# Performance work log

Measured on AMD Instinct MI355X. Metric: run time of the kernel, lower is better.

The kernel has to match this reference:

```python
import jax, jax.numpy as jnp
import numpy as np

DIM, QK, GS, DEPTH, VOCAB, ROT = 16, 128, 256, 8, 1024, 32
EPS = 1e-5


def scale_norm(x, g):
    # ScaleNorm: x / max(||x|| * dim^-0.5, eps) * g
    norm = jnp.linalg.norm(x, axis=-1, keepdims=True) * (DIM ** -0.5)
    return x / jnp.clip(norm, EPS) * g


def rotate_half(x):
    # interleaved pairs: (x0,x1,x2,x3,...) -> (-x1,x0,-x3,x2,...)
    xr = x.reshape(x.shape[:-1] + (-1, 2))
    a, b = xr[..., 0], xr[..., 1]
    return jnp.stack((-b, a), axis=-1).reshape(x.shape)


def apply_rotary(x, cos, sin):
    # rotary applied to first ROT dims only
    xr, xp = x[..., :ROT], x[..., ROT:]
    return jnp.concatenate([xr * cos + rotate_half(xr) * sin, xp], axis=-1)


def flash_layer(x, p, cos, sin, keymask, n):
    b = x.shape[0]
    normed = scale_norm(x, p['norm_g'])
    # shift_tokens: first half of channels shifted forward by one position
    xs, xp = jnp.split(normed, 2, axis=-1)
    xs = jnp.pad(xs, ((0, 0), (1, 0), (0, 0)))[:, :-1]
    normed = jnp.concatenate([xs, xp], axis=-1)
    hid = jax.nn.silu(normed @ p['Wh'] + p['bh'])  # [b,n,64]
    v, gate = jnp.split(hid, 2, axis=-1)           # each [b,n,32]
    qk = jax.nn.silu(normed @ p['Wqk'] + p['bqk'])  # [b,n,128]
    offs = qk[..., None, :] * p['gamma'] + p['beta']  # [b,n,4,128]
    quad_q, lin_q, quad_k, lin_k = [apply_rotary(offs[..., i, :], cos, sin) for i in range(4)]
    pad = (-n) % GS
    grp = lambda t: jnp.pad(t, ((0, 0), (0, pad), (0, 0))).reshape(b, -1, GS, t.shape[-1])
    quad_q, quad_k, lin_q, lin_k, vg = map(grp, (quad_q, quad_k, lin_q, lin_k, v))
    # quadratic (local, within-group) attention with ReLU^2
    sim = jnp.einsum('bgid,bgjd->bgij', quad_q, quad_k) / GS
    attn = jnp.square(jax.nn.relu(sim)) * keymask  # mask out padded keys
    quad_out = jnp.einsum('bgij,bgjd->bgid', attn, vg)
    # linear (global, across-group) attention, reduced over groups
    lin_kv = jnp.einsum('bgnd,bgne->bde', lin_k, vg) / n
    lin_out = jnp.einsum('bgnd,bde->bgne', lin_q, lin_kv)
    out = (quad_out + lin_out).reshape(b, -1, v.shape[-1])[:, :n]
    out = gate * out
    return out @ p['Wo'] + p['bo'] + x


def forward(kmer_data, token_emb, pos_scale, norm_g, Wh, bh, Wqk, bqk, gamma, beta, Wo, bo, final_g, Wl, bl, W1, b1, W2, b2):
    b, n = kmer_data.shape
    x = token_emb[kmer_data]  # [b,n,16]
    t = jnp.arange(n, dtype=jnp.float32)
    # ScaledSinuEmbedding
    inv = 1.0 / (10000.0 ** (jnp.arange(0, DIM, 2, dtype=jnp.float32) / DIM))
    sinu = t[:, None] * inv[None, :]
    pos = jnp.concatenate([jnp.sin(sinu), jnp.cos(sinu)], axis=-1) * pos_scale
    x = x + pos
    # rotary tables (dim 32, interleaved repeat)
    rinv = 1.0 / (10000.0 ** (jnp.arange(0, ROT, 2, dtype=jnp.float32) / ROT))
    rf = jnp.repeat(t[:, None] * rinv[None, :], 2, axis=-1)  # [n,32]
    cos, sin = jnp.cos(rf), jnp.sin(rf)
    # key mask for padded positions (996 -> 1024)
    pad = (-n) % GS
    keymask = jnp.pad(jnp.ones((n,), jnp.float32), (0, pad)).reshape(1, -1, 1, GS)
    for i in range(DEPTH):
        p = dict(norm_g=norm_g[i], Wh=Wh[i], bh=bh[i], Wqk=Wqk[i], bqk=bqk[i],
                 gamma=gamma[i], beta=beta[i], Wo=Wo[i], bo=bo[i])
        x = flash_layer(x, p, cos, sin, keymask, n)
    logits = scale_norm(x, final_g) @ Wl + bl  # [b,n,1024]
    h = jnp.max(logits, axis=-1)               # AdaptiveMaxPool1d(1) + Flatten -> [b,n]
    h = jax.nn.relu(h @ W1 + b1)
    return h @ W2 + b2                          # [b,1]


def setup_inputs() -> dict:
    key = jax.random.key(0)
    ks = jax.random.split(key, 12)
    r = lambda k, shape, s: jax.random.normal(k, shape, jnp.float32) * s
    return {
        'kmer_data': jax.random.randint(ks[0], (128, 996), 0, VOCAB),
        'token_emb': r(ks[1], (VOCAB, DIM), 1.0),
        'pos_scale': jnp.float32(1.0),
        'norm_g': jnp.ones((DEPTH,), jnp.float32),
        'Wh': r(ks[2], (DEPTH, DIM, 64), 0.1),
        'bh': jnp.zeros((DEPTH, 64), jnp.float32),
        'Wqk': r(ks[3], (DEPTH, DIM, QK), 0.1),
        'bqk': jnp.zeros((DEPTH, QK), jnp.float32),
        'gamma': 1.0 + r(ks[4], (DEPTH, 4, QK), 0.02),
        'beta': r(ks[5], (DEPTH, 4, QK), 0.02),
        'Wo': r(ks[6], (DEPTH, 32, DIM), 0.1),
        'bo': jnp.zeros((DEPTH, DIM), jnp.float32),
        'final_g': jnp.float32(1.0),
        'Wl': r(ks[7], (DIM, VOCAB), 0.1),
        'bl': jnp.zeros((VOCAB,), jnp.float32),
        'W1': r(ks[8], (996, 32), 0.05),
        'b1': jnp.zeros((32,), jnp.float32),
        'W2': r(ks[9], (32, 1), 0.1),
        'b2': jnp.zeros((1,), jnp.float32),
    }


def reference(kmer_data, token_emb, pos_scale, norm_g, Wh, bh, Wqk, bqk, gamma, beta, Wo, bo, final_g, Wl, bl, W1, b1, W2, b2):
    return forward(kmer_data, token_emb, pos_scale, norm_g, Wh, bh, Wqk, bqk,
                   gamma, beta, Wo, bo, final_g, Wl, bl, W1, b1, W2, b2)
```

## Files before the change

kernel.cpp:

```cpp
#include <hip/hip_runtime.h>

typedef short s16x8 __attribute__((ext_vector_type(8)));
typedef float f32x4 __attribute__((ext_vector_type(4)));

#define NB    128
#define NTOK  996
#define NPAD  1024
#define NGRP  4
#define GSZ   256
#define NLAY  8

__device__ __forceinline__ float bf2f(unsigned short u){
    unsigned int v = ((unsigned int)u) << 16;
    return __uint_as_float(v);
}
__device__ __forceinline__ unsigned short f2bf(float f){
    unsigned int x = __float_as_uint(f);
    unsigned int r = (x + 0x7fffu + ((x >> 16) & 1u)) >> 16;
    return (unsigned short)r;
}
__device__ __forceinline__ unsigned int packbf(float a, float b){
    return (unsigned int)f2bf(a) | ((unsigned int)f2bf(b) << 16);
}
__device__ __forceinline__ float silu(float v){
    return v / (1.0f + __expf(-v));
}

__device__ __forceinline__ s16x8 derive_core(const unsigned short* __restrict__ qrow, int d0,
        float4 g0, float4 g1, float4 b0, float4 b1,
        const float* __restrict__ rp, bool rot){
    uint4 u = *(const uint4*)(qrow + d0);
    float y0 = bf2f((unsigned short)(u.x & 0xffffu))*g0.x + b0.x;
    float y1 = bf2f((unsigned short)(u.x >> 16))    *g0.y + b0.y;
    float y2 = bf2f((unsigned short)(u.y & 0xffffu))*g0.z + b0.z;
    float y3 = bf2f((unsigned short)(u.y >> 16))    *g0.w + b0.w;
    float y4 = bf2f((unsigned short)(u.z & 0xffffu))*g1.x + b1.x;
    float y5 = bf2f((unsigned short)(u.z >> 16))    *g1.y + b1.y;
    float y6 = bf2f((unsigned short)(u.w & 0xffffu))*g1.z + b1.z;
    float y7 = bf2f((unsigned short)(u.w >> 16))    *g1.w + b1.w;
    if (rot){
        float4 c4 = *(const float4*)(rp);
        float4 s4 = *(const float4*)(rp + 16);
        float a;
        a = y0; y0 = a*c4.x - y1*s4.x; y1 = y1*c4.x + a*s4.x;
        a = y2; y2 = a*c4.y - y3*s4.y; y3 = y3*c4.y + a*s4.y;
        a = y4; y4 = a*c4.z - y5*s4.z; y5 = y5*c4.z + a*s4.z;
        a = y6; y6 = a*c4.w - y7*s4.w; y7 = y7*c4.w + a*s4.w;
    }
    union { unsigned int uu[4]; s16x8 s; } r;
    r.uu[0] = packbf(y0, y1);
    r.uu[1] = packbf(y2, y3);
    r.uu[2] = packbf(y4, y5);
    r.uu[3] = packbf(y6, y7);
    return r.s;
}

__global__ void k_rope(float* __restrict__ rope){
    int t = blockIdx.x * 256 + threadIdx.x;
    if (t >= NPAD) return;
    float tf = (float)t;
    #pragma unroll
    for (int i = 0; i < 16; i++){
        float inv = expf(((float)(2*i) / 32.0f) * -9.210340371976184f);
        float ang = tf * inv;
        rope[t*32 + i]      = cosf(ang);
        rope[t*32 + 16 + i] = sinf(ang);
    }
}

__global__ __launch_bounds__(256) void k_embed(const int* __restrict__ kmer,
                                               const float* __restrict__ emb,
                                               const float* __restrict__ ps,
                                               float* __restrict__ x){
    int gid = blockIdx.x * 256 + threadIdx.x;
    if (gid >= NB * NTOK) return;
    int b = gid / NTOK;
    int tt = gid - b * NTOK;
    int idx = kmer[gid];
    const float* er = emb + (size_t)idx * 16;
    float pscale = ps[0];
    float tf = (float)tt;
    float* xr = x + (size_t)gid * 16;
    #pragma unroll
    for (int i = 0; i < 8; i++){
        float inv = expf(((float)(2*i) / 16.0f) * -9.210340371976184f);
        float ang = tf * inv;
        xr[i]     = er[i]     + sinf(ang) * pscale;
        xr[8 + i] = er[8 + i] + cosf(ang) * pscale;
    }
}

__global__ __launch_bounds__(256) void k_padzero(unsigned short* __restrict__ vT){
    int rid = blockIdx.x * 256 + threadIdx.x;
    if (rid < NB * 32){
        unsigned int* vp = (unsigned int*)(vT + (size_t)rid * NPAD + NTOK);
        #pragma unroll
        for (int i = 0; i < 14; i++) vp[i] = 0u;
    }
}

__global__ __launch_bounds__(256) void k_pre(const float* __restrict__ x,
                                             const float* __restrict__ Wh, const float* __restrict__ bh,
                                             const float* __restrict__ Wqk, const float* __restrict__ bqk,
                                             const float* __restrict__ norm_g, int layer,
                                             unsigned short* __restrict__ qk,
                                             unsigned short* __restrict__ vT,
                                             unsigned short* __restrict__ gateb){
    __shared__ __align__(16) unsigned short WcT[192 * 40];
    __shared__ __align__(16) unsigned short As[256 * 40];
    int tid = threadIdx.x;
    const float* Whl = Wh  + (size_t)layer * 1024;
    const float* Wql = Wqk + (size_t)layer * 2048;
    for (int i = tid; i < 1024; i += 256){ int d = i >> 6, c = i & 63;  WcT[c*40 + d] = f2bf(Whl[i]); }
    for (int i = tid; i < 2048; i += 256){ int d = i >> 7, c = i & 127; WcT[(64 + c)*40 + d] = f2bf(Wql[i]); }
    if (tid < 192){
        int i = tid;
        float bv = (i < 64) ? bh[layer*64 + i] : bqk[layer*128 + (i - 64)];
        WcT[i*40 + 16] = f2bf(bv);
        WcT[i*40 + 17] = 0;
        unsigned int* zz = (unsigned int*)(WcT + i*40 + 18);
        #pragma unroll
        for (int k = 0; k < 7; k++) zz[k] = 0u;
    }
    int gid0 = blockIdx.x * 256;
    {
        int t = gid0 + tid;
        int b = t / NTOK, tt = t - b * NTOK;
        float g = norm_g[layer];
        const float4* xr4 = (const float4*)(x + (size_t)t * 16);
        float cur[16];
        float s2 = 0.f;
        #pragma unroll
        for (int c = 0; c < 4; c++){
            float4 v4 = xr4[c];
            cur[4*c] = v4.x; cur[4*c+1] = v4.y; cur[4*c+2] = v4.z; cur[4*c+3] = v4.w;
        }
        #pragma unroll
        for (int d = 0; d < 16; d++) s2 += cur[d]*cur[d];
        float sc = g / fmaxf(sqrtf(s2) * 0.25f, 1e-5f);
        float pv[8]; float sp = 0.f;
        #pragma unroll
        for (int d = 0; d < 8; d++) pv[d] = 0.f;
        if (tt > 0){
            const float4* xp4 = (const float4*)(x + (size_t)(t - 1) * 16);
            float prv[16]; float p2 = 0.f;
            #pragma unroll
            for (int c = 0; c < 4; c++){
                float4 v4 = xp4[c];
                prv[4*c] = v4.x; prv[4*c+1] = v4.y; prv[4*c+2] = v4.z; prv[4*c+3] = v4.w;
            }
            #pragma unroll
            for (int d = 0; d < 16; d++) p2 += prv[d]*prv[d];
            sp = g / fmaxf(sqrtf(p2) * 0.25f, 1e-5f);
            #pragma unroll
            for (int d = 0; d < 8; d++) pv[d] = prv[d];
        }
        unsigned int* dd = (unsigned int*)(As + tid * 40);
        #pragma unroll
        for (int i = 0; i < 4; i++) dd[i] = packbf(pv[2*i]*sp, pv[2*i+1]*sp);
        #pragma unroll
        for (int i = 0; i < 4; i++) dd[4 + i] = packbf(cur[8 + 2*i]*sc, cur[9 + 2*i]*sc);
        dd[8] = 0x00003f80u;
        #pragma unroll
        for (int i = 9; i < 16; i++) dd[i] = 0u;
    }
    __syncthreads();
    int w = tid >> 6, lane = tid & 63, m16 = lane & 15, quad = lane >> 4;
    s16x8 wf[12];
    #pragma unroll
    for (int mi = 0; mi < 12; mi++)
        wf[mi] = *(const s16x8*)(WcT + (mi*16 + m16)*40 + quad*8);
    f32x4 zacc = {0.f,0.f,0.f,0.f};
    #pragma unroll
    for (int nt = 0; nt < 4; nt++){
        int tloc = w*64 + nt*16 + m16;
        int t = gid0 + tloc;
        int b = t / NTOK, tt = t - b * NTOK;
        s16x8 bf = *(const s16x8*)(As + tloc*40 + quad*8);
        size_t rowq = ((size_t)b*NPAD + tt);
        #pragma unroll
        for (int mi = 0; mi < 12; mi++){
            f32x4 r = __builtin_amdgcn_mfma_f32_16x16x32_bf16(wf[mi], bf, zacc, 0, 0, 0);
            float sv[4];
            #pragma unroll
            for (int reg = 0; reg < 4; reg++) sv[reg] = silu(r[reg]);
            int wc0 = mi*16 + quad*4;
            if (mi < 2){
                #pragma unroll
                for (int reg = 0; reg < 4; reg++)
                    vT[((size_t)b*32 + wc0 + reg)*NPAD + tt] = f2bf(sv[reg]);
            } else if (mi < 4){
                *(uint2*)(gateb + rowq*32 + (wc0 - 32)) = make_uint2(packbf(sv[0],sv[1]), packbf(sv[2],sv[3]));
            } else {
                *(uint2*)(qk + rowq*128 + (wc0 - 64)) = make_uint2(packbf(sv[0],sv[1]), packbf(sv[2],sv[3]));
            }
        }
    }
}

__global__ __launch_bounds__(256) void k_linkv(const unsigned short* __restrict__ qk,
                                               const unsigned short* __restrict__ vT,
                                               const float* __restrict__ rope,
                                               const float* __restrict__ gamma, const float* __restrict__ beta,
                                               int layer, float* __restrict__ linkvp){
    __shared__ __align__(16) unsigned short LkT[2][128 * 40];
    int tid = threadIdx.x;
    int b = blockIdx.x >> 2, qt = blockIdx.x & 3;
    const float* gam = gamma + (size_t)layer * 512 + 384;
    const float* bet = beta  + (size_t)layer * 512 + 384;
    int tt = tid >> 3, dseg = (tid & 7) * 16;
    float gr[16], br[16];
    #pragma unroll
    for (int i = 0; i < 16; i++){ gr[i] = gam[dseg + i]; br[i] = bet[dseg + i]; }
    int w = tid >> 6, lane = tid & 63, m16 = lane & 15, quad = lane >> 4;
    f32x4 acc[2][2] = {{{0,0,0,0},{0,0,0,0}},{{0,0,0,0},{0,0,0,0}}};
    for (int ch = 0; ch < 8; ch++){
        unsigned short* L = LkT[ch & 1];
        {
            int t = qt*256 + ch*32 + tt;
            const uint4* s4 = (const uint4*)(qk + ((size_t)b * NPAD + t) * 128 + dseg);
            float y[16];
            #pragma unroll
            for (int c = 0; c < 2; c++){
                uint4 u = s4[c];
                unsigned int uu[4] = {u.x, u.y, u.z, u.w};
                #pragma unroll
                for (int k = 0; k < 4; k++){
                    int dl = c*8 + 2*k;
                    y[dl]   = bf2f((unsigned short)(uu[k] & 0xffffu)) * gr[dl]   + br[dl];
                    y[dl+1] = bf2f((unsigned short)(uu[k] >> 16))     * gr[dl+1] + br[dl+1];
                }
            }
            if (dseg < 32){
                const float* rp = rope + t*32 + (dseg >> 1);
                #pragma unroll
                for (int i = 0; i < 8; i++){
                    float c = rp[i], s = rp[16 + i];
                    float ya = y[2*i], yb = y[2*i+1];
                    y[2*i]   = ya*c - yb*s;
                    y[2*i+1] = yb*c + ya*s;
                }
            }
            #pragma unroll
            for (int i = 0; i < 16; i++) L[(dseg + i)*40 + tt] = f2bf(y[i]);
        }
        __syncthreads();
        int t0 = qt*256 + ch*32;
        s16x8 af0 = *(const s16x8*)(L + ((w*2)  *16 + m16)*40 + quad*8);
        s16x8 af1 = *(const s16x8*)(L + ((w*2+1)*16 + m16)*40 + quad*8);
        s16x8 bf0 = *(const s16x8*)(vT + ((size_t)b*32 + m16)*NPAD + t0 + quad*8);
        s16x8 bf1 = *(const s16x8*)(vT + ((size_t)b*32 + 16 + m16)*NPAD + t0 + quad*8);
        acc[0][0] = __builtin_amdgcn_mfma_f32_16x16x32_bf16(af0, bf0, acc[0][0], 0,0,0);
        acc[0][1] = __builtin_amdgcn_mfma_f32_16x16x32_bf16(af0, bf1, acc[0][1], 0,0,0);
        acc[1][0] = __builtin_amdgcn_mfma_f32_16x16x32_bf16(af1, bf0, acc[1][0], 0,0,0);
        acc[1][1] = __builtin_amdgcn_mfma_f32_16x16x32_bf16(af1, bf1, acc[1][1], 0,0,0);
    }
    const float invn = 1.0f / 996.0f;
    #pragma unroll
    for (int i = 0; i < 2; i++){
        #pragma unroll
        for (int j = 0; j < 2; j++){
            int e = j*16 + m16;
            #pragma unroll
            for (int reg = 0; reg < 4; reg++){
                int d = (w*2 + i)*16 + quad*4 + reg;
                linkvp[(((size_t)qt*NB + b)*32 + e)*128 + d] = acc[i][j][reg] * invn;
            }
        }
    }
}

__global__ __launch_bounds__(256) void k_lkred(const float* __restrict__ linkvp,
                                               unsigned short* __restrict__ linkvb){
    int i4 = blockIdx.x * 256 + threadIdx.x;
    size_t off = (size_t)i4 * 4;
    const float* p0 = linkvp + off;
    float4 a = *(const float4*)p0;
    float4 b = *(const float4*)(p0 + (size_t)NB*4096);
    float4 c = *(const float4*)(p0 + (size_t)2*NB*4096);
    float4 d = *(const float4*)(p0 + (size_t)3*NB*4096);
    float s0 = a.x + b.x + c.x + d.x;
    float s1 = a.y + b.y + c.y + d.y;
    float s2 = a.z + b.z + c.z + d.z;
    float s3 = a.w + b.w + c.w + d.w;
    *(uint2*)(linkvb + off) = make_uint2(packbf(s0, s1), packbf(s2, s3));
}

__device__ __forceinline__ void deriveK_chunk(unsigned short* __restrict__ Kbuf,
        const unsigned short* __restrict__ qk, int b, int tk0,
        const float* __restrict__ gK, const float* __restrict__ bK,
        const float* __restrict__ rope, int tid){
    int r = tid >> 3, seg = (tid & 7) * 16;
    int tk = tk0 + r;
    const unsigned short* krow = qk + ((size_t)b*NPAD + tk)*128 + seg;
    unsigned int* dst = (unsigned int*)(Kbuf + r*136 + seg);
    #pragma unroll
    for (int h = 0; h < 2; h++){
        uint4 u = ((const uint4*)krow)[h];
        unsigned int uu[4] = {u.x, u.y, u.z, u.w};
        float y[8];
        #pragma unroll
        for (int k = 0; k < 4; k++){
            int d = h*8 + 2*k;
            y[2*k]   = bf2f((unsigned short)(uu[k] & 0xffffu)) * gK[seg + d]     + bK[seg + d];
            y[2*k+1] = bf2f((unsigned short)(uu[k] >> 16))     * gK[seg + d + 1] + bK[seg + d + 1];
        }
        if (seg < 32){
            const float* rp = rope + tk*32 + (seg >> 1) + h*4;
            #pragma unroll
            for (int p = 0; p < 4; p++){
                float c = rp[p], s = rp[16 + p];
                float a = y[2*p], d = y[2*p+1];
                y[2*p]   = a*c - d*s;
                y[2*p+1] = d*c + a*s;
            }
        }
        #pragma unroll
        for (int k = 0; k < 4; k++) dst[h*4 + k] = packbf(y[2*k], y[2*k+1]);
    }
}

#define KD_BYTES (64*136*2)
#define PW_BYTES (8*16*72*2)
__global__ __launch_bounds__(512, 2) void k_quad(const unsigned short* __restrict__ qk,
                                              const unsigned short* __restrict__ vT,
                                              const unsigned short* __restrict__ gateb,
                                              const unsigned short* __restrict__ linkvb,
                                              const float* __restrict__ rope,
                                              const float* __restrict__ gamma, const float* __restrict__ beta,
                                              int layer,
                                              const float* __restrict__ Wo, const float* __restrict__ bo,
                                              float* __restrict__ x){
    __shared__ __align__(16) unsigned char smem[KD_BYTES + PW_BYTES];
    __shared__ float sWo[512];
    __shared__ float sbo[16];
    unsigned short* Kd = (unsigned short*)smem;
    unsigned short* Pw = (unsigned short*)(smem + KD_BYTES);
    int tid = threadIdx.x;
    int blk = blockIdx.x;
    int g = blk & 3, b = blk >> 2;
    int tg0 = g * GSZ;
    const float* gamL = gamma + (size_t)layer * 512;
    const float* betL = beta  + (size_t)layer * 512;
    sWo[tid] = Wo[layer*512 + tid];
    if (tid < 16) sbo[tid] = bo[layer*16 + tid];

    int w = tid >> 6, lane = tid & 63, m16 = lane & 15, quad = lane >> 4;

    int tqA = tg0 + w*32 + m16;
    int tqB = tqA + 16;
    const unsigned short* qrowA = qk + ((size_t)b*NPAD + tqA)*128;
    const unsigned short* qrowB = qk + ((size_t)b*NPAD + tqB)*128;
    const float* rpA = rope + tqA*32 + quad*4;
    const float* rpB = rope + tqB*32 + quad*4;
    s16x8 qf[2][4];
    #pragma unroll
    for (int ks = 0; ks < 4; ks++){
        int d0 = ks*32 + quad*8;
        float4 g0 = *(const float4*)(gamL + d0), g1 = *(const float4*)(gamL + d0 + 4);
        float4 b0 = *(const float4*)(betL + d0), b1 = *(const float4*)(betL + d0 + 4);
        bool rot = (ks == 0) && (quad < 4);
        qf[0][ks] = derive_core(qrowA, d0, g0,g1,b0,b1, rpA, rot);
        qf[1][ks] = derive_core(qrowB, d0, g0,g1,b0,b1, rpB, rot);
    }

    const float* gK = gamL + 256;
    const float* bK = betL + 256;
    f32x4 oacc[2][2] = {{{0,0,0,0},{0,0,0,0}},{{0,0,0,0},{0,0,0,0}}};
    unsigned short* myP = Pw + w*16*72;

    for (int ch = 0; ch < 4; ch++){
        __syncthreads();
        deriveK_chunk(Kd, qk, b, tg0 + ch*64, gK, bK, rope, tid);
        __syncthreads();
        #pragma unroll
        for (int i = 0; i < 2; i++){
            #pragma unroll
            for (int np = 0; np < 2; np++){
                f32x4 s0 = {0,0,0,0}, s1 = {0,0,0,0};
                #pragma unroll
                for (int ks = 0; ks < 4; ks++){
                    s16x8 kf0 = *(const s16x8*)(Kd + ((np*2  )*16 + m16)*136 + ks*32 + quad*8);
                    s16x8 kf1 = *(const s16x8*)(Kd + ((np*2+1)*16 + m16)*136 + ks*32 + quad*8);
                    s0 = __builtin_amdgcn_mfma_f32_16x16x32_bf16(qf[i][ks], kf0, s0, 0,0,0);
                    s1 = __builtin_amdgcn_mfma_f32_16x16x32_bf16(qf[i][ks], kf1, s1, 0,0,0);
                }
                #pragma unroll
                for (int j = 0; j < 2; j++){
                    int kl = (np*2 + j)*16 + m16;
                    bool kv = (tg0 + ch*64 + kl) < NTOK;
                    #pragma unroll
                    for (int reg = 0; reg < 4; reg++){
                        float a = fmaxf(j ? s1[reg] : s0[reg], 0.0f);
                        a = a * a;
                        myP[(quad*4 + reg)*72 + kl] = kv ? f2bf(a) : (unsigned short)0;
                    }
                }
            }
            #pragma unroll
            for (int ks = 0; ks < 2; ks++){
                s16x8 pa = *(const s16x8*)(myP + m16*72 + ks*32 + quad*8);
                s16x8 vf0 = *(const s16x8*)(vT + ((size_t)b*32 + m16)*NPAD + tg0 + ch*64 + ks*32 + quad*8);
                s16x8 vf1 = *(const s16x8*)(vT + ((size_t)b*32 + 16 + m16)*NPAD + tg0 + ch*64 + ks*32 + quad*8);
                oacc[i][0] = __builtin_amdgcn_mfma_f32_16x16x32_bf16(pa, vf0, oacc[i][0], 0,0,0);
                oacc[i][1] = __builtin_amdgcn_mfma_f32_16x16x32_bf16(pa, vf1, oacc[i][1], 0,0,0);
            }
        }
    }
    const float qsc = 1.0f / 65536.0f;
    #pragma unroll
    for (int i = 0; i < 2; i++)
        #pragma unroll
        for (int j = 0; j < 2; j++)
            oacc[i][j] = oacc[i][j] * qsc;
    {
        const float* gamQ = gamL + 128;
        const float* betQ = betL + 128;
        #pragma unroll
        for (int ks = 0; ks < 4; ks++){
            int d0 = ks*32 + quad*8;
            float4 g0 = *(const float4*)(gamQ + d0), g1 = *(const float4*)(gamQ + d0 + 4);
            float4 b0 = *(const float4*)(betQ + d0), b1 = *(const float4*)(betQ + d0 + 4);
            bool rot = (ks == 0) && (quad < 4);
            s16x8 lf0 = derive_core(qrowA, d0, g0,g1,b0,b1, rpA, rot);
            s16x8 lf1 = derive_core(qrowB, d0, g0,g1,b0,b1, rpB, rot);
            #pragma unroll
            for (int j = 0; j < 2; j++){
                s16x8 lb = *(const s16x8*)(linkvb + ((size_t)b*32 + j*16 + m16)*128 + ks*32 + quad*8);
                oacc[0][j] = __builtin_amdgcn_mfma_f32_16x16x32_bf16(lf0, lb, oacc[0][j], 0,0,0);
                oacc[1][j] = __builtin_amdgcn_mfma_f32_16x16x32_bf16(lf1, lb, oacc[1][j], 0,0,0);
            }
        }
    }
    __syncthreads();
    float* Obw = (float*)smem + w*1056;
    #pragma unroll
    for (int i = 0; i < 2; i++)
        #pragma unroll
        for (int j = 0; j < 2; j++)
            #pragma unroll
            for (int reg = 0; reg < 4; reg++)
                Obw[(i*16 + quad*4 + reg)*33 + j*16 + m16] = oacc[i][j][reg];
    {
        int r = lane >> 1, dp = (lane & 1) * 8;
        int p = tg0 + w*32 + r;
        if (p < NTOK){
            const unsigned short* gr = gateb + ((size_t)b*NPAD + p)*32;
            float* xr = x + ((size_t)b * NTOK + p)*16 + dp;
            float4 x0 = *(const float4*)xr;
            float4 x1 = *(const float4*)(xr + 4);
            float a[8] = { sbo[dp]+x0.x, sbo[dp+1]+x0.y, sbo[dp+2]+x0.z, sbo[dp+3]+x0.w,
                           sbo[dp+4]+x1.x, sbo[dp+5]+x1.y, sbo[dp+6]+x1.z, sbo[dp+7]+x1.w };
            #pragma unroll
            for (int eh = 0; eh < 4; eh++){
                uint4 gu = *(const uint4*)(gr + eh*8);
                unsigned int gg[4] = {gu.x, gu.y, gu.z, gu.w};
                #pragma unroll
                for (int k = 0; k < 4; k++){
                    float gv0 = bf2f((unsigned short)(gg[k] & 0xffffu));
                    float gv1 = bf2f((unsigned short)(gg[k] >> 16));
                    int e = eh*8 + 2*k;
                    float ov0 = Obw[r*33 + e] * gv0;
                    float ov1 = Obw[r*33 + e + 1] * gv1;
                    const float* wr0 = &sWo[e*16 + dp];
                    const float* wr1 = &sWo[(e+1)*16 + dp];
                    #pragma unroll
                    for (int kk = 0; kk < 8; kk++) a[kk] += ov0 * wr0[kk] + ov1 * wr1[kk];
                }
            }
            *(float4*)xr = make_float4(a[0],a[1],a[2],a[3]);
            *(float4*)(xr+4) = make_float4(a[4],a[5],a[6],a[7]);
        }
    }
}

__global__ __launch_bounds__(256) void k_head(const float* __restrict__ x,
                                              const float* __restrict__ Wl, const float* __restrict__ bl,
                                              const float* __restrict__ fg, float* __restrict__ h){
    __shared__ __align__(16) unsigned short WlT[512 * 40];
    __shared__ __align__(16) unsigned short As[64 * 40];
    int tid = threadIdx.x;
    int gid0 = blockIdx.x * 64;
    if (tid < 64){
        int t = gid0 + tid;
        const float4* xr4 = (const float4*)(x + (size_t)t * 16);
        float cur[16]; float s2 = 0.f;
        #pragma unroll
        for (int c = 0; c < 4; c++){
            float4 v4 = xr4[c];
            cur[4*c] = v4.x; cur[4*c+1] = v4.y; cur[4*c+2] = v4.z; cur[4*c+3] = v4.w;
        }
        #pragma unroll
        for (int d = 0; d < 16; d++) s2 += cur[d]*cur[d];
        float sc = fg[0] / fmaxf(sqrtf(s2) * 0.25f, 1e-5f);
        unsigned int* dd = (unsigned int*)(As + tid * 40);
        #pragma unroll
        for (int i = 0; i < 8; i++) dd[i] = packbf(cur[2*i]*sc, cur[2*i+1]*sc);
        dd[8] = 0x00003f80u;
        #pragma unroll
        for (int i = 9; i < 16; i++) dd[i] = 0u;
    }
    int w = tid >> 6, lane = tid & 63, m16 = lane & 15, quad = lane >> 4;
    float vm0 = -3e38f, vm1 = -3e38f, vm2 = -3e38f, vm3 = -3e38f;
    for (int half = 0; half < 2; half++){
        __syncthreads();
        for (int i = tid; i < 8192; i += 256){
            int d = i >> 9, c = i & 511;
            WlT[c*40 + d] = f2bf(Wl[(size_t)d*1024 + half*512 + c]);
        }
        for (int i = tid; i < 512; i += 256){
            WlT[i*40 + 16] = f2bf(bl[half*512 + i]);
            WlT[i*40 + 17] = 0;
            unsigned int* zz = (unsigned int*)(WlT + i*40 + 18);
            #pragma unroll
            for (int k = 0; k < 7; k++) zz[k] = 0u;
        }
        __syncthreads();
        s16x8 af = *(const s16x8*)(As + (w*16 + m16)*40 + quad*8);
        f32x4 zacc = {0,0,0,0};
        for (int nt = 0; nt < 32; nt++){
            s16x8 bf = *(const s16x8*)(WlT + (nt*16 + m16)*40 + quad*8);
            f32x4 r = __builtin_amdgcn_mfma_f32_16x16x32_bf16(af, bf, zacc, 0,0,0);
            vm0 = fmaxf(vm0, r[0]);
            vm1 = fmaxf(vm1, r[1]);
            vm2 = fmaxf(vm2, r[2]);
            vm3 = fmaxf(vm3, r[3]);
        }
    }
    #pragma unroll
    for (int off = 1; off < 16; off <<= 1){
        vm0 = fmaxf(vm0, __shfl_xor(vm0, off, 64));
        vm1 = fmaxf(vm1, __shfl_xor(vm1, off, 64));
        vm2 = fmaxf(vm2, __shfl_xor(vm2, off, 64));
        vm3 = fmaxf(vm3, __shfl_xor(vm3, off, 64));
    }
    if (m16 == 0){
        int t0 = gid0 + w*16 + quad*4;
        h[t0 + 0] = vm0;
        h[t0 + 1] = vm1;
        h[t0 + 2] = vm2;
        h[t0 + 3] = vm3;
    }
}

__global__ __launch_bounds__(256) void k_final(const float* __restrict__ h,
                                               const float* __restrict__ W1, const float* __restrict__ b1,
                                               const float* __restrict__ W2, const float* __restrict__ b2,
                                               float* __restrict__ out){
    int b = blockIdx.x;
    int tid = threadIdx.x;
    int j = tid & 31, part = tid >> 5;
    float acc = 0.f;
    for (int i = part; i < NTOK; i += 8)
        acc += h[(size_t)b*NTOK + i] * W1[(size_t)i*32 + j];
    __shared__ float red[8][33];
    red[part][j] = acc;
    __syncthreads();
    if (tid < 32){
        float s = b1[tid];
        #pragma unroll
        for (int p = 0; p < 8; p++) s += red[p][tid];
        s = fmaxf(s, 0.f);
        red[0][tid] = s * W2[tid];
    }
    __syncthreads();
    if (tid == 0){
        float s = b2[0];
        #pragma unroll
        for (int jj = 0; jj < 32; jj++) s += red[0][jj];
        out[b] = s;
    }
}

extern "C" void kernel_launch(void* const* d_in, const int* in_sizes, int n_in,
                              void* d_out, int out_size, void* d_ws, size_t ws_size,
                              hipStream_t stream){
    const int*   kmer  = (const int*)d_in[0];
    const float* emb   = (const float*)d_in[1];
    const float* ps    = (const float*)d_in[2];
    const float* ng    = (const float*)d_in[3];
    const float* Wh    = (const float*)d_in[4];
    const float* bh    = (const float*)d_in[5];
    const float* Wqk   = (const float*)d_in[6];
    const float* bqk   = (const float*)d_in[7];
    const float* gamma = (const float*)d_in[8];
    const float* beta  = (const float*)d_in[9];
    const float* Wo    = (const float*)d_in[10];
    const float* bo    = (const float*)d_in[11];
    const float* fg    = (const float*)d_in[12];
    const float* Wl    = (const float*)d_in[13];
    const float* bl    = (const float*)d_in[14];
    const float* W1    = (const float*)d_in[15];
    const float* b1    = (const float*)d_in[16];
    const float* W2    = (const float*)d_in[17];
    const float* b2    = (const float*)d_in[18];
    float* out = (float*)d_out;

    char* wsp = (char*)d_ws;
    float* x = (float*)wsp;                     wsp += (size_t)NB*NTOK*16*4;
    unsigned short* qk = (unsigned short*)wsp;  wsp += (size_t)NB*NPAD*128*2;
    unsigned short* vT = (unsigned short*)wsp;  wsp += (size_t)NB*32*NPAD*2;
    unsigned short* gateb = (unsigned short*)wsp; wsp += (size_t)NB*NPAD*32*2;
    float* linkvp = (float*)wsp;                wsp += (size_t)4*NB*32*128*4;
    unsigned short* linkvb = (unsigned short*)wsp; wsp += (size_t)NB*32*128*2;
    float* rope = (float*)wsp;                  wsp += (size_t)NPAD*32*4;
    float* h = (float*)wsp;                     wsp += (size_t)NB*NTOK*4;

    k_rope<<<4, 256, 0, stream>>>(rope);
    k_embed<<<(NB*NTOK + 255)/256, 256, 0, stream>>>(kmer, emb, ps, x);
    k_padzero<<<16, 256, 0, stream>>>(vT);
    for (int layer = 0; layer < NLAY; layer++){
        k_pre<<<NB*NTOK/256, 256, 0, stream>>>(x, Wh, bh, Wqk, bqk, ng, layer, qk, vT, gateb);
        k_linkv<<<NB*4, 256, 0, stream>>>(qk, vT, rope, gamma, beta, layer, linkvp);
        k_lkred<<<512, 256, 0, stream>>>(linkvp, linkvb);
        k_quad<<<NB*NGRP, 512, 0, stream>>>(qk, vT, gateb, linkvb, rope, gamma, beta, layer, Wo, bo, x);
    }
    k_head<<<NB*NTOK/64, 256, 0, stream>>>(x, Wl, bl, fg, h);
    k_final<<<NB, 256, 0, stream>>>(h, W1, b1, W2, b2, out);
}
```

Baseline: 925.3 us.

## Precompute rotated quad-K in pre-kernel and split quad attention blocks

The quad-K derivation (gamma/beta offset plus rotary) moves out of k_quad into k_pre and is written to a new global Kq buffer, so k_quad no longer recomputes K per group through LDS with block barriers. k_quad is split into two 256-thread blocks per group, each handling half of the queries, and K fragments are read straight from global memory. Each wave now computes 32 query rows against shared K loads. This adds an extra bf16 K buffer write and read per layer and more global K traffic, since both query halves reload the same K, in exchange for fewer syncs and better parallelism.

```diff
diff --git a/kernel.cpp b/kernel.cpp
--- a/kernel.cpp
+++ b/kernel.cpp
@@ -102,8 +102,11 @@
 __global__ __launch_bounds__(256) void k_pre(const float* __restrict__ x,
                                              const float* __restrict__ Wh, const float* __restrict__ bh,
                                              const float* __restrict__ Wqk, const float* __restrict__ bqk,
-                                             const float* __restrict__ norm_g, int layer,
+                                             const float* __restrict__ norm_g,
+                                             const float* __restrict__ gamma, const float* __restrict__ beta,
+                                             const float* __restrict__ rope, int layer,
                                              unsigned short* __restrict__ qk,
+                                             unsigned short* __restrict__ Kq,
                                              unsigned short* __restrict__ vT,
                                              unsigned short* __restrict__ gateb){
     __shared__ __align__(16) unsigned short WcT[192 * 40];
@@ -111,6 +114,8 @@
     int tid = threadIdx.x;
     const float* Whl = Wh  + (size_t)layer * 1024;
     const float* Wql = Wqk + (size_t)layer * 2048;
+    const float* gK = gamma + (size_t)layer * 512 + 256;
+    const float* bK = beta  + (size_t)layer * 512 + 256;
     for (int i = tid; i < 1024; i += 256){ int d = i >> 6, c = i & 63;  WcT[c*40 + d] = f2bf(Whl[i]); }
     for (int i = tid; i < 2048; i += 256){ int d = i >> 7, c = i & 127; WcT[(64 + c)*40 + d] = f2bf(Wql[i]); }
     if (tid < 192){
@@ -192,7 +197,20 @@
             } else if (mi < 4){
                 *(uint2*)(gateb + rowq*32 + (wc0 - 32)) = make_uint2(packbf(sv[0],sv[1]), packbf(sv[2],sv[3]));
             } else {
-                *(uint2*)(qk + rowq*128 + (wc0 - 64)) = make_uint2(packbf(sv[0],sv[1]), packbf(sv[2],sv[3]));
+                int qd = wc0 - 64;
+                *(uint2*)(qk + rowq*128 + qd) = make_uint2(packbf(sv[0],sv[1]), packbf(sv[2],sv[3]));
+                float y0 = sv[0]*gK[qd]   + bK[qd];
+                float y1 = sv[1]*gK[qd+1] + bK[qd+1];
+                float y2 = sv[2]*gK[qd+2] + bK[qd+2];
+                float y3 = sv[3]*gK[qd+3] + bK[qd+3];
+                if (qd < 32){
+                    const float* rp = rope + tt*32 + (qd >> 1);
+                    float c0 = rp[0], s0 = rp[16], c1 = rp[1], s1 = rp[17];
+                    float a;
+                    a = y0; y0 = a*c0 - y1*s0; y1 = y1*c0 + a*s0;
+                    a = y2; y2 = a*c1 - y3*s1; y3 = y3*c1 + a*s1;
+                }
+                *(uint2*)(Kq + rowq*128 + qd) = make_uint2(packbf(y0,y1), packbf(y2,y3));
             }
         }
     }
@@ -286,43 +304,8 @@
     *(uint2*)(linkvb + off) = make_uint2(packbf(s0, s1), packbf(s2, s3));
 }
 
-__device__ __forceinline__ void deriveK_chunk(unsigned short* __restrict__ Kbuf,
-        const unsigned short* __restrict__ qk, int b, int tk0,
-        const float* __restrict__ gK, const float* __restrict__ bK,
-        const float* __restrict__ rope, int tid){
-    int r = tid >> 3, seg = (tid & 7) * 16;
-    int tk = tk0 + r;
-    const unsigned short* krow = qk + ((size_t)b*NPAD + tk)*128 + seg;
-    unsigned int* dst = (unsigned int*)(Kbuf + r*136 + seg);
-    #pragma unroll
-    for (int h = 0; h < 2; h++){
-        uint4 u = ((const uint4*)krow)[h];
-        unsigned int uu[4] = {u.x, u.y, u.z, u.w};
-        float y[8];
-        #pragma unroll
-        for (int k = 0; k < 4; k++){
-            int d = h*8 + 2*k;
-            y[2*k]   = bf2f((unsigned short)(uu[k] & 0xffffu)) * gK[seg + d]     + bK[seg + d];
-            y[2*k+1] = bf2f((unsigned short)(uu[k] >> 16))     * gK[seg + d + 1] + bK[seg + d + 1];
-        }
-        if (seg < 32){
-            const float* rp = rope + tk*32 + (seg >> 1) + h*4;
-            #pragma unroll
-            for (int p = 0; p < 4; p++){
-                float c = rp[p], s = rp[16 + p];
-                float a = y[2*p], d = y[2*p+1];
-                y[2*p]   = a*c - d*s;
-                y[2*p+1] = d*c + a*s;
-            }
-        }
-        #pragma unroll
-        for (int k = 0; k < 4; k++) dst[h*4 + k] = packbf(y[2*k], y[2*k+1]);
-    }
-}
-
-#define KD_BYTES (64*136*2)
-#define PW_BYTES (8*16*72*2)
-__global__ __launch_bounds__(512, 2) void k_quad(const unsigned short* __restrict__ qk,
+__global__ __launch_bounds__(256, 2) void k_quad(const unsigned short* __restrict__ qk,
+                                              const unsigned short* __restrict__ Kq,
                                               const unsigned short* __restrict__ vT,
                                               const unsigned short* __restrict__ gateb,
                                               const unsigned short* __restrict__ linkvb,
@@ -331,23 +314,22 @@
                                               int layer,
                                               const float* __restrict__ Wo, const float* __restrict__ bo,
                                               float* __restrict__ x){
-    __shared__ __align__(16) unsigned char smem[KD_BYTES + PW_BYTES];
+    __shared__ __align__(16) unsigned short Pw[4 * 32 * 72];
     __shared__ float sWo[512];
     __shared__ float sbo[16];
-    unsigned short* Kd = (unsigned short*)smem;
-    unsigned short* Pw = (unsigned short*)(smem + KD_BYTES);
     int tid = threadIdx.x;
     int blk = blockIdx.x;
-    int g = blk & 3, b = blk >> 2;
+    int qh = blk & 1, g = (blk >> 1) & 3, b = blk >> 3;
     int tg0 = g * GSZ;
     const float* gamL = gamma + (size_t)layer * 512;
     const float* betL = beta  + (size_t)layer * 512;
     sWo[tid] = Wo[layer*512 + tid];
+    sWo[256 + tid] = Wo[layer*512 + 256 + tid];
     if (tid < 16) sbo[tid] = bo[layer*16 + tid];
 
     int w = tid >> 6, lane = tid & 63, m16 = lane & 15, quad = lane >> 4;
 
-    int tqA = tg0 + w*32 + m16;
+    int tqA = tg0 + qh*128 + w*32 + m16;
     int tqB = tqA + 16;
     const unsigned short* qrowA = qk + ((size_t)b*NPAD + tqA)*128;
     const unsigned short* qrowB = qk + ((size_t)b*NPAD + tqB)*128;
@@ -364,42 +346,43 @@
         qf[1][ks] = derive_core(qrowB, d0, g0,g1,b0,b1, rpB, rot);
     }
 
-    const float* gK = gamL + 256;
-    const float* bK = betL + 256;
     f32x4 oacc[2][2] = {{{0,0,0,0},{0,0,0,0}},{{0,0,0,0},{0,0,0,0}}};
-    unsigned short* myP = Pw + w*16*72;
+    unsigned short* myP = Pw + w*32*72;
 
     for (int ch = 0; ch < 4; ch++){
-        __syncthreads();
-        deriveK_chunk(Kd, qk, b, tg0 + ch*64, gK, bK, rope, tid);
-        __syncthreads();
+        const unsigned short* Kbase = Kq + ((size_t)b*NPAD + tg0 + ch*64)*128;
+        #pragma unroll
+        for (int np = 0; np < 2; np++){
+            f32x4 sA0 = {0,0,0,0}, sA1 = {0,0,0,0}, sB0 = {0,0,0,0}, sB1 = {0,0,0,0};
+            #pragma unroll
+            for (int ks = 0; ks < 4; ks++){
+                s16x8 kf0 = *(const s16x8*)(Kbase + ((size_t)(np*32 + m16))*128 + ks*32 + quad*8);
+                s16x8 kf1 = *(const s16x8*)(Kbase + ((size_t)(np*32 + 16 + m16))*128 + ks*32 + quad*8);
+                sA0 = __builtin_amdgcn_mfma_f32_16x16x32_bf16(qf[0][ks], kf0, sA0, 0,0,0);
+                sA1 = __builtin_amdgcn_mfma_f32_16x16x32_bf16(qf[0][ks], kf1, sA1, 0,0,0);
+                sB0 = __builtin_amdgcn_mfma_f32_16x16x32_bf16(qf[1][ks], kf0, sB0, 0,0,0);
+                sB1 = __builtin_amdgcn_mfma_f32_16x16x32_bf16(qf[1][ks], kf1, sB1, 0,0,0);
+            }
+            #pragma unroll
+            for (int j = 0; j < 2; j++){
+                int kl = (np*2 + j)*16 + m16;
+                bool kv = (tg0 + ch*64 + kl) < NTOK;
+                #pragma unroll
+                for (int reg = 0; reg < 4; reg++){
+                    float a0 = fmaxf(j ? sA1[reg] : sA0[reg], 0.0f);
+                    float a1 = fmaxf(j ? sB1[reg] : sB0[reg], 0.0f);
+                    a0 = a0 * a0;
+                    a1 = a1 * a1;
+                    myP[(quad*4 + reg)*72 + kl]        = kv ? f2bf(a0) : (unsigned short)0;
+                    myP[(16 + quad*4 + reg)*72 + kl]   = kv ? f2bf(a1) : (unsigned short)0;
+                }
+            }
+        }
         #pragma unroll
         for (int i = 0; i < 2; i++){
             #pragma unroll
-            for (int np = 0; np < 2; np++){
-                f32x4 s0 = {0,0,0,0}, s1 = {0,0,0,0};
-                #pragma unroll
-                for (int ks = 0; ks < 4; ks++){
-                    s16x8 kf0 = *(const s16x8*)(Kd + ((np*2  )*16 + m16)*136 + ks*32 + quad*8);
-                    s16x8 kf1 = *(const s16x8*)(Kd + ((np*2+1)*16 + m16)*136 + ks*32 + quad*8);
-                    s0 = __builtin_amdgcn_mfma_f32_16x16x32_bf16(qf[i][ks], kf0, s0, 0,0,0);
-                    s1 = __builtin_amdgcn_mfma_f32_16x16x32_bf16(qf[i][ks], kf1, s1, 0,0,0);
-                }
-                #pragma unroll
-                for (int j = 0; j < 2; j++){
-                    int kl = (np*2 + j)*16 + m16;
-                    bool kv = (tg0 + ch*64 + kl) < NTOK;
-                    #pragma unroll
-                    for (int reg = 0; reg < 4; reg++){
-                        float a = fmaxf(j ? s1[reg] : s0[reg], 0.0f);
-                        a = a * a;
-                        myP[(quad*4 + reg)*72 + kl] = kv ? f2bf(a) : (unsigned short)0;
-                    }
-                }
-            }
-            #pragma unroll
             for (int ks = 0; ks < 2; ks++){
-                s16x8 pa = *(const s16x8*)(myP + m16*72 + ks*32 + quad*8);
+                s16x8 pa = *(const s16x8*)(myP + (i*16 + m16)*72 + ks*32 + quad*8);
                 s16x8 vf0 = *(const s16x8*)(vT + ((size_t)b*32 + m16)*NPAD + tg0 + ch*64 + ks*32 + quad*8);
                 s16x8 vf1 = *(const s16x8*)(vT + ((size_t)b*32 + 16 + m16)*NPAD + tg0 + ch*64 + ks*32 + quad*8);
                 oacc[i][0] = __builtin_amdgcn_mfma_f32_16x16x32_bf16(pa, vf0, oacc[i][0], 0,0,0);
@@ -432,8 +415,7 @@
             }
         }
     }
-    __syncthreads();
-    float* Obw = (float*)smem + w*1056;
+    float* Obw = (float*)myP;
     #pragma unroll
     for (int i = 0; i < 2; i++)
         #pragma unroll
@@ -441,9 +423,10 @@
             #pragma unroll
             for (int reg = 0; reg < 4; reg++)
                 Obw[(i*16 + quad*4 + reg)*33 + j*16 + m16] = oacc[i][j][reg];
+    __syncthreads();
     {
         int r = lane >> 1, dp = (lane & 1) * 8;
-        int p = tg0 + w*32 + r;
+        int p = tg0 + qh*128 + w*32 + r;
         if (p < NTOK){
             const unsigned short* gr = gateb + ((size_t)b*NPAD + p)*32;
             float* xr = x + ((size_t)b * NTOK + p)*16 + dp;
@@ -599,6 +582,7 @@
     char* wsp = (char*)d_ws;
     float* x = (float*)wsp;                     wsp += (size_t)NB*NTOK*16*4;
     unsigned short* qk = (unsigned short*)wsp;  wsp += (size_t)NB*NPAD*128*2;
+    unsigned short* Kq = (unsigned short*)wsp;  wsp += (size_t)NB*NPAD*128*2;
     unsigned short* vT = (unsigned short*)wsp;  wsp += (size_t)NB*32*NPAD*2;
     unsigned short* gateb = (unsigned short*)wsp; wsp += (size_t)NB*NPAD*32*2;
     float* linkvp = (float*)wsp;                wsp += (size_t)4*NB*32*128*4;
@@ -610,10 +594,10 @@
     k_embed<<<(NB*NTOK + 255)/256, 256, 0, stream>>>(kmer, emb, ps, x);
     k_padzero<<<16, 256, 0, stream>>>(vT);
     for (int layer = 0; layer < NLAY; layer++){
-        k_pre<<<NB*NTOK/256, 256, 0, stream>>>(x, Wh, bh, Wqk, bqk, ng, layer, qk, vT, gateb);
+        k_pre<<<NB*NTOK/256, 256, 0, stream>>>(x, Wh, bh, Wqk, bqk, ng, gamma, beta, rope, layer, qk, Kq, vT, gateb);
         k_linkv<<<NB*4, 256, 0, stream>>>(qk, vT, rope, gamma, beta, layer, linkvp);
         k_lkred<<<512, 256, 0, stream>>>(linkvp, linkvb);
-        k_quad<<<NB*NGRP, 512, 0, stream>>>(qk, vT, gateb, linkvb, rope, gamma, beta, layer, Wo, bo, x);
+        k_quad<<<NB*NGRP*2, 256, 0, stream>>>(qk, Kq, vT, gateb, linkvb, rope, gamma, beta, layer, Wo, bo, x);
     }
     k_head<<<NB*NTOK/64, 256, 0, stream>>>(x, Wl, bl, fg, h);
     k_final<<<NB, 256, 0, stream>>>(h, W1, b1, W2, b2, out);
```

Measured after the change: 1.167 ms. 26.2% more time.

## Fuse linear-KV partial reduction into quad kernel and share shifted norms in k_pre

Applied to the files above, without the earlier changes.

Drops the separate k_lkred launch. Each k_quad block now sums the four fp32 partial linear-KV tiles for its batch, converts them to bf16 in shared memory and reads MFMA operands from there instead of from global. In k_pre, each thread writes its own normalized first-half channels to shared memory, and the next thread reads them for the token shift instead of reloading and renormalizing the previous token; only thread 0 still goes to global. This saves one launch per layer and the redundant loads and norm math, but each quad block (4 per batch) repeats the partial reduction and uses more shared memory, which could lower occupancy.

```diff
diff --git a/kernel.cpp b/kernel.cpp
--- a/kernel.cpp
+++ b/kernel.cpp
@@ -108,6 +108,7 @@
                                              unsigned short* __restrict__ gateb){
     __shared__ __align__(16) unsigned short WcT[192 * 40];
     __shared__ __align__(16) unsigned short As[256 * 40];
+    __shared__ unsigned int nrm[256][4];
     int tid = threadIdx.x;
     const float* Whl = Wh  + (size_t)layer * 1024;
     const float* Wql = Wqk + (size_t)layer * 2048;
@@ -123,10 +124,11 @@
         for (int k = 0; k < 7; k++) zz[k] = 0u;
     }
     int gid0 = blockIdx.x * 256;
+    int t = gid0 + tid;
+    int b = t / NTOK, tt = t - b * NTOK;
+    float g = norm_g[layer];
+    unsigned int* dd = (unsigned int*)(As + tid * 40);
     {
-        int t = gid0 + tid;
-        int b = t / NTOK, tt = t - b * NTOK;
-        float g = norm_g[layer];
         const float4* xr4 = (const float4*)(x + (size_t)t * 16);
         float cur[16];
         float s2 = 0.f;
@@ -138,31 +140,34 @@
         #pragma unroll
         for (int d = 0; d < 16; d++) s2 += cur[d]*cur[d];
         float sc = g / fmaxf(sqrtf(s2) * 0.25f, 1e-5f);
-        float pv[8]; float sp = 0.f;
-        #pragma unroll
-        for (int d = 0; d < 8; d++) pv[d] = 0.f;
-        if (tt > 0){
-            const float4* xp4 = (const float4*)(x + (size_t)(t - 1) * 16);
-            float prv[16]; float p2 = 0.f;
-            #pragma unroll
-            for (int c = 0; c < 4; c++){
-                float4 v4 = xp4[c];
-                prv[4*c] = v4.x; prv[4*c+1] = v4.y; prv[4*c+2] = v4.z; prv[4*c+3] = v4.w;
-            }
-            #pragma unroll
-            for (int d = 0; d < 16; d++) p2 += prv[d]*prv[d];
-            sp = g / fmaxf(sqrtf(p2) * 0.25f, 1e-5f);
-            #pragma unroll
-            for (int d = 0; d < 8; d++) pv[d] = prv[d];
-        }
-        unsigned int* dd = (unsigned int*)(As + tid * 40);
-        #pragma unroll
-        for (int i = 0; i < 4; i++) dd[i] = packbf(pv[2*i]*sp, pv[2*i+1]*sp);
+        #pragma unroll
+        for (int i = 0; i < 4; i++) nrm[tid][i] = packbf(cur[2*i]*sc, cur[2*i+1]*sc);
         #pragma unroll
         for (int i = 0; i < 4; i++) dd[4 + i] = packbf(cur[8 + 2*i]*sc, cur[9 + 2*i]*sc);
         dd[8] = 0x00003f80u;
         #pragma unroll
         for (int i = 9; i < 16; i++) dd[i] = 0u;
+    }
+    __syncthreads();
+    if (tt == 0){
+        #pragma unroll
+        for (int i = 0; i < 4; i++) dd[i] = 0u;
+    } else if (tid > 0){
+        #pragma unroll
+        for (int i = 0; i < 4; i++) dd[i] = nrm[tid - 1][i];
+    } else {
+        const float4* xp4 = (const float4*)(x + (size_t)(t - 1) * 16);
+        float prv[16]; float p2 = 0.f;
+        #pragma unroll
+        for (int c = 0; c < 4; c++){
+            float4 v4 = xp4[c];
+            prv[4*c] = v4.x; prv[4*c+1] = v4.y; prv[4*c+2] = v4.z; prv[4*c+3] = v4.w;
+        }
+        #pragma unroll
+        for (int d = 0; d < 16; d++) p2 += prv[d]*prv[d];
+        float sp = g / fmaxf(sqrtf(p2) * 0.25f, 1e-5f);
+        #pragma unroll
+        for (int i = 0; i < 4; i++) dd[i] = packbf(prv[2*i]*sp, prv[2*i+1]*sp);
     }
     __syncthreads();
     int w = tid >> 6, lane = tid & 63, m16 = lane & 15, quad = lane >> 4;
@@ -174,10 +179,10 @@
     #pragma unroll
     for (int nt = 0; nt < 4; nt++){
         int tloc = w*64 + nt*16 + m16;
-        int t = gid0 + tloc;
-        int b = t / NTOK, tt = t - b * NTOK;
+        int tg = gid0 + tloc;
+        int bb = tg / NTOK, ttt = tg - bb * NTOK;
         s16x8 bf = *(const s16x8*)(As + tloc*40 + quad*8);
-        size_t rowq = ((size_t)b*NPAD + tt);
+        size_t rowq = ((size_t)bb*NPAD + ttt);
         #pragma unroll
         for (int mi = 0; mi < 12; mi++){
             f32x4 r = __builtin_amdgcn_mfma_f32_16x16x32_bf16(wf[mi], bf, zacc, 0, 0, 0);
@@ -188,7 +193,7 @@
             if (mi < 2){
                 #pragma unroll
                 for (int reg = 0; reg < 4; reg++)
-                    vT[((size_t)b*32 + wc0 + reg)*NPAD + tt] = f2bf(sv[reg]);
+                    vT[((size_t)bb*32 + wc0 + reg)*NPAD + ttt] = f2bf(sv[reg]);
             } else if (mi < 4){
                 *(uint2*)(gateb + rowq*32 + (wc0 - 32)) = make_uint2(packbf(sv[0],sv[1]), packbf(sv[2],sv[3]));
             } else {
@@ -270,68 +275,19 @@
     }
 }
 
-__global__ __launch_bounds__(256) void k_lkred(const float* __restrict__ linkvp,
-                                               unsigned short* __restrict__ linkvb){
-    int i4 = blockIdx.x * 256 + threadIdx.x;
-    size_t off = (size_t)i4 * 4;
-    const float* p0 = linkvp + off;
-    float4 a = *(const float4*)p0;
-    float4 b = *(const float4*)(p0 + (size_t)NB*4096);
-    float4 c = *(const float4*)(p0 + (size_t)2*NB*4096);
-    float4 d = *(const float4*)(p0 + (size_t)3*NB*4096);
-    float s0 = a.x + b.x + c.x + d.x;
-    float s1 = a.y + b.y + c.y + d.y;
-    float s2 = a.z + b.z + c.z + d.z;
-    float s3 = a.w + b.w + c.w + d.w;
-    *(uint2*)(linkvb + off) = make_uint2(packbf(s0, s1), packbf(s2, s3));
-}
-
-__device__ __forceinline__ void deriveK_chunk(unsigned short* __restrict__ Kbuf,
-        const unsigned short* __restrict__ qk, int b, int tk0,
-        const float* __restrict__ gK, const float* __restrict__ bK,
-        const float* __restrict__ rope, int tid){
-    int r = tid >> 3, seg = (tid & 7) * 16;
-    int tk = tk0 + r;
-    const unsigned short* krow = qk + ((size_t)b*NPAD + tk)*128 + seg;
-    unsigned int* dst = (unsigned int*)(Kbuf + r*136 + seg);
-    #pragma unroll
-    for (int h = 0; h < 2; h++){
-        uint4 u = ((const uint4*)krow)[h];
-        unsigned int uu[4] = {u.x, u.y, u.z, u.w};
-        float y[8];
-        #pragma unroll
-        for (int k = 0; k < 4; k++){
-            int d = h*8 + 2*k;
-            y[2*k]   = bf2f((unsigned short)(uu[k] & 0xffffu)) * gK[seg + d]     + bK[seg + d];
-            y[2*k+1] = bf2f((unsigned short)(uu[k] >> 16))     * gK[seg + d + 1] + bK[seg + d + 1];
-        }
-        if (seg < 32){
-            const float* rp = rope + tk*32 + (seg >> 1) + h*4;
-            #pragma unroll
-            for (int p = 0; p < 4; p++){
-                float c = rp[p], s = rp[16 + p];
-                float a = y[2*p], d = y[2*p+1];
-                y[2*p]   = a*c - d*s;
-                y[2*p+1] = d*c + a*s;
-            }
-        }
-        #pragma unroll
-        for (int k = 0; k < 4; k++) dst[h*4 + k] = packbf(y[2*k], y[2*k+1]);
-    }
-}
-
 #define KD_BYTES (64*136*2)
 #define PW_BYTES (8*16*72*2)
 __global__ __launch_bounds__(512, 2) void k_quad(const unsigned short* __restrict__ qk,
                                               const unsigned short* __restrict__ vT,
                                               const unsigned short* __restrict__ gateb,
-                                              const unsigned short* __restrict__ linkvb,
+                                              const float* __restrict__ linkvp,
                                               const float* __restrict__ rope,
                                               const float* __restrict__ gamma, const float* __restrict__ beta,
                                               int layer,
                                               const float* __restrict__ Wo, const float* __restrict__ bo,
                                               float* __restrict__ x){
     __shared__ __align__(16) unsigned char smem[KD_BYTES + PW_BYTES];
+    __shared__ __align__(16) unsigned short LkBs[32 * 136];
     __shared__ float sWo[512];
     __shared__ float sbo[16];
     unsigned short* Kd = (unsigned short*)smem;
@@ -371,7 +327,36 @@
 
     for (int ch = 0; ch < 4; ch++){
         __syncthreads();
-        deriveK_chunk(Kd, qk, b, tg0 + ch*64, gK, bK, rope, tid);
+        {
+            int r = tid >> 3, seg = (tid & 7) * 16;
+            int tk = tg0 + ch*64 + r;
+            const unsigned short* krow = qk + ((size_t)b*NPAD + tk)*128 + seg;
+            unsigned int* dst = (unsigned int*)(Kd + r*136 + seg);
+            #pragma unroll
+            for (int h = 0; h < 2; h++){
+                uint4 u = ((const uint4*)krow)[h];
+                unsigned int uu[4] = {u.x, u.y, u.z, u.w};
+                float y[8];
+                #pragma unroll
+                for (int k = 0; k < 4; k++){
+                    int d = h*8 + 2*k;
+                    y[2*k]   = bf2f((unsigned short)(uu[k] & 0xffffu)) * gK[seg + d]     + bK[seg + d];
+                    y[2*k+1] = bf2f((unsigned short)(uu[k] >> 16))     * gK[seg + d + 1] + bK[seg + d + 1];
+                }
+                if (seg < 32){
+                    const float* rp = rope + tk*32 + (seg >> 1) + h*4;
+                    #pragma unroll
+                    for (int p = 0; p < 4; p++){
+                        float c = rp[p], s = rp[16 + p];
+                        float a = y[2*p], d = y[2*p+1];
+                        y[2*p]   = a*c - d*s;
+                        y[2*p+1] = d*c + a*s;
+                    }
+                }
+                #pragma unroll
+                for (int k = 0; k < 4; k++) dst[h*4 + k] = packbf(y[2*k], y[2*k+1]);
+            }
+        }
         __syncthreads();
         #pragma unroll
         for (int i = 0; i < 2; i++){
@@ -414,6 +399,24 @@
         for (int j = 0; j < 2; j++)
             oacc[i][j] = oacc[i][j] * qsc;
     {
+        int e = tid >> 4, dbase = (tid & 15) * 8;
+        float s[8];
+        #pragma unroll
+        for (int k = 0; k < 8; k++) s[k] = 0.f;
+        #pragma unroll
+        for (int part = 0; part < 4; part++){
+            const float* src = linkvp + (((size_t)part*NB + b)*32 + e)*128 + dbase;
+            float4 u0 = *(const float4*)src;
+            float4 u1 = *(const float4*)(src + 4);
+            s[0]+=u0.x; s[1]+=u0.y; s[2]+=u0.z; s[3]+=u0.w;
+            s[4]+=u1.x; s[5]+=u1.y; s[6]+=u1.z; s[7]+=u1.w;
+        }
+        unsigned int* dst = (unsigned int*)(LkBs + e*136 + dbase);
+        #pragma unroll
+        for (int k = 0; k < 4; k++) dst[k] = packbf(s[2*k], s[2*k+1]);
+    }
+    __syncthreads();
+    {
         const float* gamQ = gamL + 128;
         const float* betQ = betL + 128;
         #pragma unroll
@@ -426,13 +429,12 @@
             s16x8 lf1 = derive_core(qrowB, d0, g0,g1,b0,b1, rpB, rot);
             #pragma unroll
             for (int j = 0; j < 2; j++){
-                s16x8 lb = *(const s16x8*)(linkvb + ((size_t)b*32 + j*16 + m16)*128 + ks*32 + quad*8);
+                s16x8 lb = *(const s16x8*)(LkBs + (j*16 + m16)*136 + ks*32 + quad*8);
                 oacc[0][j] = __builtin_amdgcn_mfma_f32_16x16x32_bf16(lf0, lb, oacc[0][j], 0,0,0);
                 oacc[1][j] = __builtin_amdgcn_mfma_f32_16x16x32_bf16(lf1, lb, oacc[1][j], 0,0,0);
             }
         }
     }
-    __syncthreads();
     float* Obw = (float*)smem + w*1056;
     #pragma unroll
     for (int i = 0; i < 2; i++)
@@ -602,7 +604,6 @@
     unsigned short* vT = (unsigned short*)wsp;  wsp += (size_t)NB*32*NPAD*2;
     unsigned short* gateb = (unsigned short*)wsp; wsp += (size_t)NB*NPAD*32*2;
     float* linkvp = (float*)wsp;                wsp += (size_t)4*NB*32*128*4;
-    unsigned short* linkvb = (unsigned short*)wsp; wsp += (size_t)NB*32*128*2;
     float* rope = (float*)wsp;                  wsp += (size_t)NPAD*32*4;
     float* h = (float*)wsp;                     wsp += (size_t)NB*NTOK*4;
 
@@ -612,8 +613,7 @@
     for (int layer = 0; layer < NLAY; layer++){
         k_pre<<<NB*NTOK/256, 256, 0, stream>>>(x, Wh, bh, Wqk, bqk, ng, layer, qk, vT, gateb);
         k_linkv<<<NB*4, 256, 0, stream>>>(qk, vT, rope, gamma, beta, layer, linkvp);
-        k_lkred<<<512, 256, 0, stream>>>(linkvp, linkvb);
-        k_quad<<<NB*NGRP, 512, 0, stream>>>(qk, vT, gateb, linkvb, rope, gamma, beta, layer, Wo, bo, x);
+        k_quad<<<NB*NGRP, 512, 0, stream>>>(qk, vT, gateb, linkvp, rope, gamma, beta, layer, Wo, bo, x);
     }
     k_head<<<NB*NTOK/64, 256, 0, stream>>>(x, Wl, bl, fg, h);
     k_final<<<NB, 256, 0, stream>>>(h, W1, b1, W2, b2, out);
```

Measured after the change: 912.0 us. Within noise of the previous version (-1.4%).
